# Optimization experiments

Hardware: AMD Instinct MI355X
Metric: run time of the kernel (lower is better)

The kernel has to match this reference:

```python
import jax, jax.numpy as jnp
import numpy as np
import math

HEAD_SIZE = 128
N_EMBED = 2048
B, T = 4, 4096
TOP_K_RATIO = 0.1


def setup_inputs() -> dict:
    key = jax.random.key(0)
    k1, k2, k3, k4 = jax.random.split(key, 4)
    index = jax.random.normal(k1, (B, T, N_EMBED), dtype=jnp.float32)
    s = 1.0 / math.sqrt(N_EMBED)
    Wq = jax.random.normal(k2, (N_EMBED, HEAD_SIZE), dtype=jnp.float32) * s
    Wk = jax.random.normal(k3, (N_EMBED, HEAD_SIZE), dtype=jnp.float32) * s
    Wv = jax.random.normal(k4, (N_EMBED, HEAD_SIZE), dtype=jnp.float32) * s
    return {"index": index, "Wq": Wq, "Wk": Wk, "Wv": Wv}


def reference(index, Wq, Wk, Wv):
    # memory = index (self-attention case)
    Bv, Tv, _ = index.shape
    top_k = int(TOP_K_RATIO * Tv)  # 409

    q = index @ Wq  # [B, T, D]
    k = index @ Wk
    v = index @ Wv

    q_norms = jnp.linalg.norm(q, axis=-1)  # [B, T]
    _, top_idx = jax.lax.top_k(q_norms, top_k)  # [B, K]

    idx = top_idx[..., None]  # [B, K, 1]
    q_topk = jnp.take_along_axis(q, idx, axis=1)  # [B, K, D]
    k_topk = jnp.take_along_axis(k, idx, axis=1)
    v_topk = jnp.take_along_axis(v, idx, axis=1)

    w = jnp.einsum('bid,bjd->bij', q_topk, k_topk) / math.sqrt(HEAD_SIZE)
    # eval mode: no causal mask (only applied in training), dropout = identity
    w = jax.nn.softmax(w, axis=-1)  # stable softmax (internal max subtraction)
    out_topk = w @ v_topk  # [B, K, D]

    batch_idx = jnp.arange(Bv)[:, None]  # [B, 1]
    output = jnp.zeros((Bv, Tv, HEAD_SIZE), dtype=out_topk.dtype)
    output = output.at[batch_idx, top_idx].add(out_topk)  # scatter_add (indices unique)
    return output
```

## Files before the change

### kernel.cpp

```cpp
#include <hip/hip_runtime.h>
#include <hip/hip_bf16.h>

#define NB 4
#define NT 4096
#define NC 2048
#define ND 128
#define NK 409
#define KPAD 416
#define NM (NB * NK)

typedef __attribute__((ext_vector_type(8))) short short8;
typedef __attribute__((ext_vector_type(4))) float f32x4;

union S8U { short8 v; ushort u[8]; };

__device__ __forceinline__ void split2(float x, ushort& h, ushort& l) {
    union { float f; unsigned u; } a; a.f = x;
    unsigned r = a.u + 0x7FFFu + ((a.u >> 16) & 1u);
    h = (ushort)(r >> 16);
    union { unsigned u; float f; } hb; hb.u = ((unsigned)h) << 16;
    float res = x - hb.f;
    union { float f; unsigned u; } b; b.f = res;
    unsigned r2 = b.u + 0x7FFFu + ((b.u >> 16) & 1u);
    l = (ushort)(r2 >> 16);
}

__device__ __forceinline__ uint4 pack8(const ushort* s) {
    uint4 v;
    v.x = (unsigned)s[0] | ((unsigned)s[1] << 16);
    v.y = (unsigned)s[2] | ((unsigned)s[3] << 16);
    v.z = (unsigned)s[4] | ((unsigned)s[5] << 16);
    v.w = (unsigned)s[6] | ((unsigned)s[7] << 16);
    return v;
}

__device__ __forceinline__ int slotOf(int n, int lq) {
    return n * 4 + ((lq + (n >> 1)) & 3);
}

__global__ __launch_bounds__(256) void bconv_tiles(
    const float* __restrict__ W, ushort* __restrict__ Bt)
{
    const int kt = blockIdx.x;
    const int t = threadIdx.x;
    const int n = t & 127;
    const int lq0 = (t >> 7) * 2;
    #pragma unroll
    for (int e = 0; e < 2; ++e) {
        int lq = lq0 + e;
        ushort h[8], l[8];
        #pragma unroll
        for (int j = 0; j < 8; ++j) {
            float x = W[(size_t)(kt * 32 + lq * 8 + j) * ND + n];
            split2(x, h[j], l[j]);
        }
        int slot = slotOf(n, lq);
        *(uint4*)&Bt[((size_t)(kt * 2 + 0) * 512 + slot) * 8] = pack8(h);
        *(uint4*)&Bt[((size_t)(kt * 2 + 1) * 512 + slot) * 8] = pack8(l);
    }
}

#define QSTEP(BHC, BLC, BHN, BLN, KT)                                         \
    {                                                                         \
        short8 ah, al;                                                        \
        {                                                                     \
            S8U H, L;                                                         \
            float xs[8] = {fa0.x, fa0.y, fa0.z, fa0.w,                        \
                           fa1.x, fa1.y, fa1.z, fa1.w};                       \
            _Pragma("unroll")                                                 \
            for (int j = 0; j < 8; ++j) split2(xs[j], H.u[j], L.u[j]);        \
            ah = H.v; al = L.v;                                               \
        }                                                                     \
        const int ktn = ((KT) + 1 < KITER) ? (KT) + 1 : (KT);                 \
        const ushort* gbn = Bt + (size_t)(kt0 + ktn) * 8192;                  \
        _Pragma("unroll")                                                     \
        for (int ni = 0; ni < 8; ++ni) {                                      \
            BHN[ni] = *(const short8*)(gbn + boff[ni]);                       \
            BLN[ni] = *(const short8*)(gbn + 4096 + boff[ni]);                \
        }                                                                     \
        fa0 = *(const float4*)(arow + ktn * 32);                              \
        fa1 = *(const float4*)(arow + ktn * 32 + 4);                          \
        _Pragma("unroll")                                                     \
        for (int ni = 0; ni < 8; ++ni) {                                      \
            acc[ni] = __builtin_amdgcn_mfma_f32_16x16x32_bf16(ah, BHC[ni], acc[ni], 0, 0, 0); \
            acc[ni] = __builtin_amdgcn_mfma_f32_16x16x32_bf16(ah, BLC[ni], acc[ni], 0, 0, 0); \
            acc[ni] = __builtin_amdgcn_mfma_f32_16x16x32_bf16(al, BHC[ni], acc[ni], 0, 0, 0); \
        }                                                                     \
    }

#define QSPLIT 2
__global__ __launch_bounds__(512, 4) void qgemm_v7(
    const float* __restrict__ A, const ushort* __restrict__ Bt,
    float* __restrict__ q1, float* __restrict__ q2)
{
    __shared__ __align__(16) float RED[4][64][32];

    const int tid = threadIdx.x;
    const int w = tid >> 6, lane = tid & 63;
    const int rg = w & 3, kh = w >> 2;
    const int lrow = lane & 15, lq = lane >> 4;
    const int m0 = blockIdx.x * 64;
    const int KITER = 16;
    const int kt0 = (blockIdx.y * 2 + kh) * 16;
    const int kb = blockIdx.y * 1024 + kh * 512;

    const float* arow = A + (size_t)(m0 + rg * 16 + lrow) * NC + kb + lq * 8;

    int boff[8];
    #pragma unroll
    for (int ni = 0; ni < 8; ++ni)
        boff[ni] = slotOf(ni * 16 + lrow, lq) * 8;

    f32x4 acc[8];
    #pragma unroll
    for (int i = 0; i < 8; ++i) acc[i] = (f32x4){0.f, 0.f, 0.f, 0.f};

    short8 bhA[8], blA[8], bhB[8], blB[8];
    {
        const ushort* gb = Bt + (size_t)kt0 * 8192;
        #pragma unroll
        for (int ni = 0; ni < 8; ++ni) {
            bhA[ni] = *(const short8*)(gb + boff[ni]);
            blA[ni] = *(const short8*)(gb + 4096 + boff[ni]);
        }
    }
    float4 fa0 = *(const float4*)(arow + 0);
    float4 fa1 = *(const float4*)(arow + 4);

    for (int kt = 0; kt < KITER; kt += 2) {
        QSTEP(bhA, blA, bhB, blB, kt);
        QSTEP(bhB, blB, bhA, blA, kt + 1);
    }

    if (kh == 1) {
        #pragma unroll
        for (int c = 0; c < 8; ++c) {
            int ch = (c + lane) & 7;
            *(f32x4*)&RED[rg][lane][ch * 4] = acc[ch];
        }
    }
    __syncthreads();
    if (kh == 0) {
        #pragma unroll
        for (int c = 0; c < 8; ++c) {
            int ch = (c + lane) & 7;
            f32x4 o = *(const f32x4*)&RED[rg][lane][ch * 4];
            acc[ch][0] += o[0]; acc[ch][1] += o[1];
            acc[ch][2] += o[2]; acc[ch][3] += o[3];
        }
        float* __restrict__ qd = blockIdx.y ? q2 : q1;
        #pragma unroll
        for (int ni = 0; ni < 8; ++ni) {
            const int col = ni * 16 + lrow;
            #pragma unroll
            for (int r = 0; r < 4; ++r) {
                const int grow = m0 + rg * 16 + lq * 4 + r;
                qd[(size_t)grow * ND + col] = acc[ni][r];
            }
        }
    }
}

#define KVSPLIT 8
__global__ __launch_bounds__(256) void kvgemm_v5(
    const float* __restrict__ X, const ushort* __restrict__ Bkt,
    const ushort* __restrict__ Bvt, const int* __restrict__ topi,
    float* __restrict__ ktop, float* __restrict__ vtop)
{
    const int tid = threadIdx.x;
    const int w = tid >> 6, lane = tid & 63;
    const int lrow = lane & 15, lq = lane >> 4;
    const int m0 = blockIdx.x * 64;
    const int KITER = (NC / KVSPLIT) / 32;
    const int kt0 = blockIdx.y * KITER;
    const int kb = blockIdx.y * (NC / KVSPLIT);
    const ushort* __restrict__ Bt = blockIdx.z ? Bvt : Bkt;

    const int gi = m0 + w * 16 + lrow;
    const int giC = gi < NM ? gi : NM - 1;
    const int b = giC / NK, ii = giC % NK;
    const int src = topi[b * KPAD + ii];
    const float* arow = X + ((size_t)b * NT + src) * NC + kb + lq * 8;

    int boff[8];
    #pragma unroll
    for (int ni = 0; ni < 8; ++ni)
        boff[ni] = slotOf(ni * 16 + lrow, lq) * 8;

    f32x4 acc[8];
    #pragma unroll
    for (int i = 0; i < 8; ++i) acc[i] = (f32x4){0.f, 0.f, 0.f, 0.f};

    short8 bhA[8], blA[8], bhB[8], blB[8];
    {
        const ushort* gb = Bt + (size_t)kt0 * 8192;
        #pragma unroll
        for (int ni = 0; ni < 8; ++ni) {
            bhA[ni] = *(const short8*)(gb + boff[ni]);
            blA[ni] = *(const short8*)(gb + 4096 + boff[ni]);
        }
    }
    float4 fa0 = *(const float4*)(arow + 0);
    float4 fa1 = *(const float4*)(arow + 4);

    for (int kt = 0; kt < KITER; kt += 2) {
        QSTEP(bhA, blA, bhB, blB, kt);
        QSTEP(bhB, blB, bhA, blA, kt + 1);
    }

    float* __restrict__ dst = blockIdx.z ? vtop : ktop;
    #pragma unroll
    for (int ni = 0; ni < 8; ++ni) {
        const int col = ni * 16 + lrow;
        #pragma unroll
        for (int r = 0; r < 4; ++r) {
            const int grow = m0 + w * 16 + lq * 4 + r;
            if (grow < NM)
                atomicAdd(&dst[(size_t)grow * ND + col], acc[ni][r]);
        }
    }
}

__global__ __launch_bounds__(256) void qnorm_kernel(
    float* __restrict__ q1, const float* __restrict__ q2, float* __restrict__ qn)
{
    const int wv = (blockIdx.x * 256 + threadIdx.x) >> 6;
    const int lane = threadIdx.x & 63;
    float* r1 = q1 + (size_t)wv * ND;
    const float* r2 = q2 + (size_t)wv * ND;
    float a = r1[lane] + r2[lane];
    float b = r1[lane + 64] + r2[lane + 64];
    r1[lane] = a;
    r1[lane + 64] = b;
    float s = a * a + b * b;
    #pragma unroll
    for (int off = 32; off > 0; off >>= 1) s += __shfl_xor(s, off);
    if (lane == 0) qn[wv] = sqrtf(s);
}

__global__ __launch_bounds__(256) void topk_kernel(
    const float* __restrict__ qn, int* __restrict__ topi, int* __restrict__ cnt)
{
    __shared__ int rs[4][64];
    const int b = blockIdx.y;
    const int is = threadIdx.x & 63;
    const int i = blockIdx.x * 64 + is;
    const int chunk = threadIdx.x >> 6;
    const float vi = qn[(size_t)b * NT + i];
    const float4* qv = (const float4*)(qn + (size_t)b * NT + chunk * 1024);
    int rank = 0;
    #pragma unroll 4
    for (int j4 = 0; j4 < 256; ++j4) {
        float4 v = qv[j4];
        int j = chunk * 1024 + j4 * 4;
        rank += (v.x > vi || (v.x == vi && (j + 0) < i)) ? 1 : 0;
        rank += (v.y > vi || (v.y == vi && (j + 1) < i)) ? 1 : 0;
        rank += (v.z > vi || (v.z == vi && (j + 2) < i)) ? 1 : 0;
        rank += (v.w > vi || (v.w == vi && (j + 3) < i)) ? 1 : 0;
    }
    rs[chunk][is] = rank;
    __syncthreads();
    if (threadIdx.x < 64) {
        int rk = rs[0][threadIdx.x] + rs[1][threadIdx.x] + rs[2][threadIdx.x] + rs[3][threadIdx.x];
        if (rk < NK) {
            int p = atomicAdd(&cnt[b], 1);
            topi[b * KPAD + p] = blockIdx.x * 64 + threadIdx.x;
        }
    }
}

__global__ __launch_bounds__(256) void attn_kernel(
    const float* __restrict__ q, const float* __restrict__ ktop,
    const float* __restrict__ vtop, const int* __restrict__ topi,
    float* __restrict__ out)
{
    __shared__ float qs[ND];
    __shared__ float ss[KPAD];
    __shared__ float red[256];
    __shared__ float pv[2][ND];
    const int bi = blockIdx.x;
    const int b = bi / NK, i = bi % NK;
    const int t = threadIdx.x;
    const int row = topi[b * KPAD + i];
    if (t < ND) qs[t] = q[((size_t)b * NT + row) * ND + t];
    __syncthreads();

    const float scale = 0.08838834764831844f;
    float mymax = -1e30f;
    #pragma unroll
    for (int rep = 0; rep < 2; ++rep) {
        int j = t + rep * 256;
        if (j < NK) {
            const float4* kr = (const float4*)(ktop + ((size_t)b * NK + j) * ND);
            const float4* q4 = (const float4*)qs;
            float s = 0.f;
            #pragma unroll
            for (int dd = 0; dd < 32; ++dd) {
                float4 a = q4[dd], kv = kr[dd];
                s += a.x * kv.x + a.y * kv.y + a.z * kv.z + a.w * kv.w;
            }
            s *= scale;
            ss[j] = s;
            mymax = fmaxf(mymax, s);
        }
    }
    red[t] = mymax;
    __syncthreads();
    for (int off = 128; off > 0; off >>= 1) {
        if (t < off) red[t] = fmaxf(red[t], red[t + off]);
        __syncthreads();
    }
    const float mx = red[0];
    __syncthreads();

    float mysum = 0.f;
    #pragma unroll
    for (int rep = 0; rep < 2; ++rep) {
        int j = t + rep * 256;
        if (j < NK) {
            float p = __expf(ss[j] - mx);
            ss[j] = p;
            mysum += p;
        }
    }
    red[t] = mysum;
    __syncthreads();
    for (int off = 128; off > 0; off >>= 1) {
        if (t < off) red[t] += red[t + off];
        __syncthreads();
    }
    const float inv = 1.f / red[0];

    const int col = t & (ND - 1), half = t >> 7;
    float o = 0.f;
    #pragma unroll 4
    for (int j = half; j < NK; j += 2)
        o = fmaf(ss[j], vtop[((size_t)b * NK + j) * ND + col], o);
    pv[half][col] = o;
    __syncthreads();
    if (t < ND)
        out[((size_t)b * NT + row) * ND + t] = (pv[0][t] + pv[1][t]) * inv;
}

extern "C" void kernel_launch(void* const* d_in, const int* in_sizes, int n_in,
                              void* d_out, int out_size, void* d_ws, size_t ws_size,
                              hipStream_t stream)
{
    const float* index = (const float*)d_in[0];
    const float* Wq = (const float*)d_in[1];
    const float* Wk = (const float*)d_in[2];
    const float* Wv = (const float*)d_in[3];
    float* out = (float*)d_out;

    char* ws = (char*)d_ws;
    float*  q1   = (float*)(ws);
    float*  qn   = (float*)(ws + 8388608);
    int*    topi = (int*)  (ws + 8454144);
    int*    cnt  = (int*)  (ws + 8462336);
    ushort* Bqt  = (ushort*)(ws + 8462592);
    float*  ktop = (float*)(ws + 8462592);
    float*  vtop = (float*)(ws + 9300224);

    float*  q2  = (float*)d_out;
    ushort* Bkt = (ushort*)d_out;
    ushort* Bvt = (ushort*)((char*)d_out + 1048576);

    hipMemsetAsync(cnt, 0, NB * sizeof(int), stream);

    bconv_tiles<<<dim3(64), dim3(256), 0, stream>>>(Wq, Bqt);
    qgemm_v7<<<dim3(NB * NT / 64, QSPLIT), dim3(512), 0, stream>>>(index, Bqt, q1, q2);
    qnorm_kernel<<<dim3(NB * NT / 4), dim3(256), 0, stream>>>(q1, q2, qn);
    topk_kernel<<<dim3(NT / 64, NB), dim3(256), 0, stream>>>(qn, topi, cnt);
    bconv_tiles<<<dim3(64), dim3(256), 0, stream>>>(Wk, Bkt);
    bconv_tiles<<<dim3(64), dim3(256), 0, stream>>>(Wv, Bvt);
    hipMemsetAsync(ktop, 0, 2 * 837632, stream);
    kvgemm_v5<<<dim3((NM + 63) / 64, KVSPLIT, 2), dim3(256), 0, stream>>>(
        index, Bkt, Bvt, topi, ktop, vtop);
    hipMemsetAsync(d_out, 0, (size_t)out_size * sizeof(float), stream);
    attn_kernel<<<dim3(NM), dim3(256), 0, stream>>>(q1, ktop, vtop, topi, out);
}
```

Baseline: 396.1 us.

## Split GEMM tiles across N halves instead of K halves, dropping LDS reduction

The Q and KV GEMM kernels now assign waves to 32-row by 64-column tiles, splitting the N dimension across waves instead of splitting K within a block. This removes the shared-memory reduction and __syncthreads in the Q GEMM, and halves the per-wave B register footprint. The cost is that each A row fragment (fp32 loaded from global and split into bf16 hi/lo) is now loaded and converted twice, once per N-half wave. Block count doubles with smaller blocks.

```diff
diff --git a/kernel.cpp b/kernel.cpp
--- a/kernel.cpp
+++ b/kernel.cpp
@@ -74,14 +74,14 @@
         const int ktn = ((KT) + 1 < KITER) ? (KT) + 1 : (KT);                 \
         const ushort* gbn = Bt + (size_t)(kt0 + ktn) * 8192;                  \
         _Pragma("unroll")                                                     \
-        for (int ni = 0; ni < 8; ++ni) {                                      \
+        for (int ni = 0; ni < 4; ++ni) {                                      \
             BHN[ni] = *(const short8*)(gbn + boff[ni]);                       \
             BLN[ni] = *(const short8*)(gbn + 4096 + boff[ni]);                \
         }                                                                     \
         fa0 = *(const float4*)(arow + ktn * 32);                              \
         fa1 = *(const float4*)(arow + ktn * 32 + 4);                          \
         _Pragma("unroll")                                                     \
-        for (int ni = 0; ni < 8; ++ni) {                                      \
+        for (int ni = 0; ni < 4; ++ni) {                                      \
             acc[ni] = __builtin_amdgcn_mfma_f32_16x16x32_bf16(ah, BHC[ni], acc[ni], 0, 0, 0); \
             acc[ni] = __builtin_amdgcn_mfma_f32_16x16x32_bf16(ah, BLC[ni], acc[ni], 0, 0, 0); \
             acc[ni] = __builtin_amdgcn_mfma_f32_16x16x32_bf16(al, BHC[ni], acc[ni], 0, 0, 0); \
@@ -89,37 +89,35 @@
     }
 
 #define QSPLIT 2
-__global__ __launch_bounds__(512, 4) void qgemm_v7(
+__global__ __launch_bounds__(256) void qgemm_v9(
     const float* __restrict__ A, const ushort* __restrict__ Bt,
     float* __restrict__ q1, float* __restrict__ q2)
 {
-    __shared__ __align__(16) float RED[4][64][32];
-
     const int tid = threadIdx.x;
     const int w = tid >> 6, lane = tid & 63;
-    const int rg = w & 3, kh = w >> 2;
+    const int rg = w & 1, nh = w >> 1;
     const int lrow = lane & 15, lq = lane >> 4;
-    const int m0 = blockIdx.x * 64;
-    const int KITER = 16;
-    const int kt0 = (blockIdx.y * 2 + kh) * 16;
-    const int kb = blockIdx.y * 1024 + kh * 512;
+    const int m0 = blockIdx.x * 32;
+    const int KITER = (NC / QSPLIT) / 32;
+    const int kt0 = blockIdx.y * KITER;
+    const int kb = blockIdx.y * (NC / QSPLIT);
 
     const float* arow = A + (size_t)(m0 + rg * 16 + lrow) * NC + kb + lq * 8;
 
-    int boff[8];
-    #pragma unroll
-    for (int ni = 0; ni < 8; ++ni)
-        boff[ni] = slotOf(ni * 16 + lrow, lq) * 8;
-
-    f32x4 acc[8];
-    #pragma unroll
-    for (int i = 0; i < 8; ++i) acc[i] = (f32x4){0.f, 0.f, 0.f, 0.f};
-
-    short8 bhA[8], blA[8], bhB[8], blB[8];
+    int boff[4];
+    #pragma unroll
+    for (int ni = 0; ni < 4; ++ni)
+        boff[ni] = slotOf(nh * 64 + ni * 16 + lrow, lq) * 8;
+
+    f32x4 acc[4];
+    #pragma unroll
+    for (int i = 0; i < 4; ++i) acc[i] = (f32x4){0.f, 0.f, 0.f, 0.f};
+
+    short8 bhA[4], blA[4], bhB[4], blB[4];
     {
         const ushort* gb = Bt + (size_t)kt0 * 8192;
         #pragma unroll
-        for (int ni = 0; ni < 8; ++ni) {
+        for (int ni = 0; ni < 4; ++ni) {
             bhA[ni] = *(const short8*)(gb + boff[ni]);
             blA[ni] = *(const short8*)(gb + 4096 + boff[ni]);
         }
@@ -132,70 +130,54 @@
         QSTEP(bhB, blB, bhA, blA, kt + 1);
     }
 
-    if (kh == 1) {
-        #pragma unroll
-        for (int c = 0; c < 8; ++c) {
-            int ch = (c + lane) & 7;
-            *(f32x4*)&RED[rg][lane][ch * 4] = acc[ch];
-        }
-    }
-    __syncthreads();
-    if (kh == 0) {
-        #pragma unroll
-        for (int c = 0; c < 8; ++c) {
-            int ch = (c + lane) & 7;
-            f32x4 o = *(const f32x4*)&RED[rg][lane][ch * 4];
-            acc[ch][0] += o[0]; acc[ch][1] += o[1];
-            acc[ch][2] += o[2]; acc[ch][3] += o[3];
-        }
-        float* __restrict__ qd = blockIdx.y ? q2 : q1;
-        #pragma unroll
-        for (int ni = 0; ni < 8; ++ni) {
-            const int col = ni * 16 + lrow;
-            #pragma unroll
-            for (int r = 0; r < 4; ++r) {
-                const int grow = m0 + rg * 16 + lq * 4 + r;
-                qd[(size_t)grow * ND + col] = acc[ni][r];
-            }
+    float* __restrict__ qd = blockIdx.y ? q2 : q1;
+    #pragma unroll
+    for (int ni = 0; ni < 4; ++ni) {
+        const int col = nh * 64 + ni * 16 + lrow;
+        #pragma unroll
+        for (int r = 0; r < 4; ++r) {
+            const int grow = m0 + rg * 16 + lq * 4 + r;
+            qd[(size_t)grow * ND + col] = acc[ni][r];
         }
     }
 }
 
 #define KVSPLIT 8
-__global__ __launch_bounds__(256) void kvgemm_v5(
+__global__ __launch_bounds__(256) void kvgemm_v9(
     const float* __restrict__ X, const ushort* __restrict__ Bkt,
     const ushort* __restrict__ Bvt, const int* __restrict__ topi,
     float* __restrict__ ktop, float* __restrict__ vtop)
 {
     const int tid = threadIdx.x;
     const int w = tid >> 6, lane = tid & 63;
+    const int rg = w & 1, nh = w >> 1;
     const int lrow = lane & 15, lq = lane >> 4;
-    const int m0 = blockIdx.x * 64;
+    const int m0 = blockIdx.x * 32;
     const int KITER = (NC / KVSPLIT) / 32;
     const int kt0 = blockIdx.y * KITER;
     const int kb = blockIdx.y * (NC / KVSPLIT);
     const ushort* __restrict__ Bt = blockIdx.z ? Bvt : Bkt;
 
-    const int gi = m0 + w * 16 + lrow;
+    const int gi = m0 + rg * 16 + lrow;
     const int giC = gi < NM ? gi : NM - 1;
     const int b = giC / NK, ii = giC % NK;
     const int src = topi[b * KPAD + ii];
     const float* arow = X + ((size_t)b * NT + src) * NC + kb + lq * 8;
 
-    int boff[8];
-    #pragma unroll
-    for (int ni = 0; ni < 8; ++ni)
-        boff[ni] = slotOf(ni * 16 + lrow, lq) * 8;
-
-    f32x4 acc[8];
-    #pragma unroll
-    for (int i = 0; i < 8; ++i) acc[i] = (f32x4){0.f, 0.f, 0.f, 0.f};
-
-    short8 bhA[8], blA[8], bhB[8], blB[8];
+    int boff[4];
+    #pragma unroll
+    for (int ni = 0; ni < 4; ++ni)
+        boff[ni] = slotOf(nh * 64 + ni * 16 + lrow, lq) * 8;
+
+    f32x4 acc[4];
+    #pragma unroll
+    for (int i = 0; i < 4; ++i) acc[i] = (f32x4){0.f, 0.f, 0.f, 0.f};
+
+    short8 bhA[4], blA[4], bhB[4], blB[4];
     {
         const ushort* gb = Bt + (size_t)kt0 * 8192;
         #pragma unroll
-        for (int ni = 0; ni < 8; ++ni) {
+        for (int ni = 0; ni < 4; ++ni) {
             bhA[ni] = *(const short8*)(gb + boff[ni]);
             blA[ni] = *(const short8*)(gb + 4096 + boff[ni]);
         }
@@ -210,11 +192,11 @@
 
     float* __restrict__ dst = blockIdx.z ? vtop : ktop;
     #pragma unroll
-    for (int ni = 0; ni < 8; ++ni) {
-        const int col = ni * 16 + lrow;
+    for (int ni = 0; ni < 4; ++ni) {
+        const int col = nh * 64 + ni * 16 + lrow;
         #pragma unroll
         for (int r = 0; r < 4; ++r) {
-            const int grow = m0 + w * 16 + lq * 4 + r;
+            const int grow = m0 + rg * 16 + lq * 4 + r;
             if (grow < NM)
                 atomicAdd(&dst[(size_t)grow * ND + col], acc[ni][r]);
         }
@@ -368,13 +350,13 @@
     hipMemsetAsync(cnt, 0, NB * sizeof(int), stream);
 
     bconv_tiles<<<dim3(64), dim3(256), 0, stream>>>(Wq, Bqt);
-    qgemm_v7<<<dim3(NB * NT / 64, QSPLIT), dim3(512), 0, stream>>>(index, Bqt, q1, q2);
+    qgemm_v9<<<dim3(NB * NT / 32, QSPLIT), dim3(256), 0, stream>>>(index, Bqt, q1, q2);
     qnorm_kernel<<<dim3(NB * NT / 4), dim3(256), 0, stream>>>(q1, q2, qn);
     topk_kernel<<<dim3(NT / 64, NB), dim3(256), 0, stream>>>(qn, topi, cnt);
     bconv_tiles<<<dim3(64), dim3(256), 0, stream>>>(Wk, Bkt);
     bconv_tiles<<<dim3(64), dim3(256), 0, stream>>>(Wv, Bvt);
     hipMemsetAsync(ktop, 0, 2 * 837632, stream);
-    kvgemm_v5<<<dim3((NM + 63) / 64, KVSPLIT, 2), dim3(256), 0, stream>>>(
+    kvgemm_v9<<<dim3((NM + 31) / 32, KVSPLIT, 2), dim3(256), 0, stream>>>(
         index, Bkt, Bvt, topi, ktop, vtop);
     hipMemsetAsync(d_out, 0, (size_t)out_size * sizeof(float), stream);
     attn_kernel<<<dim3(NM), dim3(256), 0, stream>>>(q1, ktop, vtop, topi, out);
```

Measured after the change: 389.5 us. Within noise of the previous version (-1.7%).

## Drop intra-block K-split in Q GEMM and issue A loads before B loads

Applied to the files above, without the earlier changes.

The Q projection kernel moves from 512-thread blocks, where two wave groups split the K range and reduce through shared memory, to 256-thread blocks in which each wave runs the full 1024-wide K half on its own. This removes the LDS reduction and the __syncthreads, at the cost of a longer serial K loop per wave with the same grid size. The shared pipelining macro also now issues the fp32 A-row prefetch ahead of the B-tile loads, so the activation stream, which is the longer-latency load, starts earlier. This applies to both the Q and K/V GEMMs.

```diff
diff --git a/kernel.cpp b/kernel.cpp
--- a/kernel.cpp
+++ b/kernel.cpp
@@ -72,14 +72,14 @@
             ah = H.v; al = L.v;                                               \
         }                                                                     \
         const int ktn = ((KT) + 1 < KITER) ? (KT) + 1 : (KT);                 \
+        fa0 = *(const float4*)(arow + ktn * 32);        \
+        fa1 = *(const float4*)(arow + ktn * 32 + 4);                          \
         const ushort* gbn = Bt + (size_t)(kt0 + ktn) * 8192;                  \
         _Pragma("unroll")                                                     \
         for (int ni = 0; ni < 8; ++ni) {                                      \
             BHN[ni] = *(const short8*)(gbn + boff[ni]);                       \
             BLN[ni] = *(const short8*)(gbn + 4096 + boff[ni]);                \
         }                                                                     \
-        fa0 = *(const float4*)(arow + ktn * 32);                              \
-        fa1 = *(const float4*)(arow + ktn * 32 + 4);                          \
         _Pragma("unroll")                                                     \
         for (int ni = 0; ni < 8; ++ni) {                                      \
             acc[ni] = __builtin_amdgcn_mfma_f32_16x16x32_bf16(ah, BHC[ni], acc[ni], 0, 0, 0); \
@@ -89,22 +89,19 @@
     }
 
 #define QSPLIT 2
-__global__ __launch_bounds__(512, 4) void qgemm_v7(
+__global__ __launch_bounds__(256) void qgemm_v11(
     const float* __restrict__ A, const ushort* __restrict__ Bt,
     float* __restrict__ q1, float* __restrict__ q2)
 {
-    __shared__ __align__(16) float RED[4][64][32];
-
     const int tid = threadIdx.x;
     const int w = tid >> 6, lane = tid & 63;
-    const int rg = w & 3, kh = w >> 2;
     const int lrow = lane & 15, lq = lane >> 4;
     const int m0 = blockIdx.x * 64;
-    const int KITER = 16;
-    const int kt0 = (blockIdx.y * 2 + kh) * 16;
-    const int kb = blockIdx.y * 1024 + kh * 512;
-
-    const float* arow = A + (size_t)(m0 + rg * 16 + lrow) * NC + kb + lq * 8;
+    const int KITER = (NC / QSPLIT) / 32;
+    const int kt0 = blockIdx.y * KITER;
+    const int kb = blockIdx.y * (NC / QSPLIT);
+
+    const float* arow = A + (size_t)(m0 + w * 16 + lrow) * NC + kb + lq * 8;
 
     int boff[8];
     #pragma unroll
@@ -115,6 +112,8 @@
     #pragma unroll
     for (int i = 0; i < 8; ++i) acc[i] = (f32x4){0.f, 0.f, 0.f, 0.f};
 
+    float4 fa0 = *(const float4*)(arow + 0);
+    float4 fa1 = *(const float4*)(arow + 4);
     short8 bhA[8], blA[8], bhB[8], blB[8];
     {
         const ushort* gb = Bt + (size_t)kt0 * 8192;
@@ -124,45 +123,26 @@
             blA[ni] = *(const short8*)(gb + 4096 + boff[ni]);
         }
     }
-    float4 fa0 = *(const float4*)(arow + 0);
-    float4 fa1 = *(const float4*)(arow + 4);
 
     for (int kt = 0; kt < KITER; kt += 2) {
         QSTEP(bhA, blA, bhB, blB, kt);
         QSTEP(bhB, blB, bhA, blA, kt + 1);
     }
 
-    if (kh == 1) {
-        #pragma unroll
-        for (int c = 0; c < 8; ++c) {
-            int ch = (c + lane) & 7;
-            *(f32x4*)&RED[rg][lane][ch * 4] = acc[ch];
-        }
-    }
-    __syncthreads();
-    if (kh == 0) {
-        #pragma unroll
-        for (int c = 0; c < 8; ++c) {
-            int ch = (c + lane) & 7;
-            f32x4 o = *(const f32x4*)&RED[rg][lane][ch * 4];
-            acc[ch][0] += o[0]; acc[ch][1] += o[1];
-            acc[ch][2] += o[2]; acc[ch][3] += o[3];
-        }
-        float* __restrict__ qd = blockIdx.y ? q2 : q1;
-        #pragma unroll
-        for (int ni = 0; ni < 8; ++ni) {
-            const int col = ni * 16 + lrow;
-            #pragma unroll
-            for (int r = 0; r < 4; ++r) {
-                const int grow = m0 + rg * 16 + lq * 4 + r;
-                qd[(size_t)grow * ND + col] = acc[ni][r];
-            }
+    float* __restrict__ qd = blockIdx.y ? q2 : q1;
+    #pragma unroll
+    for (int ni = 0; ni < 8; ++ni) {
+        const int col = ni * 16 + lrow;
+        #pragma unroll
+        for (int r = 0; r < 4; ++r) {
+            const int grow = m0 + w * 16 + lq * 4 + r;
+            qd[(size_t)grow * ND + col] = acc[ni][r];
         }
     }
 }
 
 #define KVSPLIT 8
-__global__ __launch_bounds__(256) void kvgemm_v5(
+__global__ __launch_bounds__(256) void kvgemm_v11(
     const float* __restrict__ X, const ushort* __restrict__ Bkt,
     const ushort* __restrict__ Bvt, const int* __restrict__ topi,
     float* __restrict__ ktop, float* __restrict__ vtop)
@@ -191,6 +171,8 @@
     #pragma unroll
     for (int i = 0; i < 8; ++i) acc[i] = (f32x4){0.f, 0.f, 0.f, 0.f};
 
+    float4 fa0 = *(const float4*)(arow + 0);
+    float4 fa1 = *(const float4*)(arow + 4);
     short8 bhA[8], blA[8], bhB[8], blB[8];
     {
         const ushort* gb = Bt + (size_t)kt0 * 8192;
@@ -200,8 +182,6 @@
             blA[ni] = *(const short8*)(gb + 4096 + boff[ni]);
         }
     }
-    float4 fa0 = *(const float4*)(arow + 0);
-    float4 fa1 = *(const float4*)(arow + 4);
 
     for (int kt = 0; kt < KITER; kt += 2) {
         QSTEP(bhA, blA, bhB, blB, kt);
@@ -368,13 +348,13 @@
     hipMemsetAsync(cnt, 0, NB * sizeof(int), stream);
 
     bconv_tiles<<<dim3(64), dim3(256), 0, stream>>>(Wq, Bqt);
-    qgemm_v7<<<dim3(NB * NT / 64, QSPLIT), dim3(512), 0, stream>>>(index, Bqt, q1, q2);
+    qgemm_v11<<<dim3(NB * NT / 64, QSPLIT), dim3(256), 0, stream>>>(index, Bqt, q1, q2);
     qnorm_kernel<<<dim3(NB * NT / 4), dim3(256), 0, stream>>>(q1, q2, qn);
     topk_kernel<<<dim3(NT / 64, NB), dim3(256), 0, stream>>>(qn, topi, cnt);
     bconv_tiles<<<dim3(64), dim3(256), 0, stream>>>(Wk, Bkt);
     bconv_tiles<<<dim3(64), dim3(256), 0, stream>>>(Wv, Bvt);
     hipMemsetAsync(ktop, 0, 2 * 837632, stream);
-    kvgemm_v5<<<dim3((NM + 63) / 64, KVSPLIT, 2), dim3(256), 0, stream>>>(
+    kvgemm_v11<<<dim3((NM + 63) / 64, KVSPLIT, 2), dim3(256), 0, stream>>>(
         index, Bkt, Bvt, topi, ktop, vtop);
     hipMemsetAsync(d_out, 0, (size_t)out_size * sizeof(float), stream);
     attn_kernel<<<dim3(NM), dim3(256), 0, stream>>>(q1, ktop, vtop, topi, out);
```

New measurement: 369.7 us. -6.7%, faster.

## Swap split-K strategies between Q and KV GEMMs and fuse K/V weight conversion

Applied to the files above, without the earlier changes.

The Q projection GEMM drops its in-block two-wave-group K split and LDS reduction and runs as a plain 256-thread kernel that splits K across two grid slices. The gathered K/V GEMM moves the opposite way: a 512-thread block splits K internally and reduces through LDS, and the grid split drops from 8 to 4, which halves the number of global atomicAdds. The two K and V weight-conversion launches are merged into one 2D launch. The A-row loads are also issued before the B-tile loads inside the pipeline step.

```diff
diff --git a/kernel.cpp b/kernel.cpp
--- a/kernel.cpp
+++ b/kernel.cpp
@@ -38,11 +38,9 @@
     return n * 4 + ((lq + (n >> 1)) & 3);
 }
 
-__global__ __launch_bounds__(256) void bconv_tiles(
-    const float* __restrict__ W, ushort* __restrict__ Bt)
-{
-    const int kt = blockIdx.x;
-    const int t = threadIdx.x;
+__device__ __forceinline__ void bconv_body(
+    const float* __restrict__ W, ushort* __restrict__ Bt, int kt, int t)
+{
     const int n = t & 127;
     const int lq0 = (t >> 7) * 2;
     #pragma unroll
@@ -58,6 +56,21 @@
         *(uint4*)&Bt[((size_t)(kt * 2 + 0) * 512 + slot) * 8] = pack8(h);
         *(uint4*)&Bt[((size_t)(kt * 2 + 1) * 512 + slot) * 8] = pack8(l);
     }
+}
+
+__global__ __launch_bounds__(256) void bconv_tiles(
+    const float* __restrict__ W, ushort* __restrict__ Bt)
+{
+    bconv_body(W, Bt, blockIdx.x, threadIdx.x);
+}
+
+__global__ __launch_bounds__(256) void bconv2_tiles(
+    const float* __restrict__ Wk, const float* __restrict__ Wv,
+    ushort* __restrict__ Bkt, ushort* __restrict__ Bvt)
+{
+    const float* W = blockIdx.y ? Wv : Wk;
+    ushort* Bt = blockIdx.y ? Bvt : Bkt;
+    bconv_body(W, Bt, blockIdx.x, threadIdx.x);
 }
 
 #define QSTEP(BHC, BLC, BHN, BLN, KT)                                         \
@@ -72,14 +85,14 @@
             ah = H.v; al = L.v;                                               \
         }                                                                     \
         const int ktn = ((KT) + 1 < KITER) ? (KT) + 1 : (KT);                 \
+        fa0 = *(const float4*)(arow + ktn * 32);                              \
+        fa1 = *(const float4*)(arow + ktn * 32 + 4);                          \
         const ushort* gbn = Bt + (size_t)(kt0 + ktn) * 8192;                  \
         _Pragma("unroll")                                                     \
         for (int ni = 0; ni < 8; ++ni) {                                      \
             BHN[ni] = *(const short8*)(gbn + boff[ni]);                       \
             BLN[ni] = *(const short8*)(gbn + 4096 + boff[ni]);                \
         }                                                                     \
-        fa0 = *(const float4*)(arow + ktn * 32);                              \
-        fa1 = *(const float4*)(arow + ktn * 32 + 4);                          \
         _Pragma("unroll")                                                     \
         for (int ni = 0; ni < 8; ++ni) {                                      \
             acc[ni] = __builtin_amdgcn_mfma_f32_16x16x32_bf16(ah, BHC[ni], acc[ni], 0, 0, 0); \
@@ -89,9 +102,63 @@
     }
 
 #define QSPLIT 2
-__global__ __launch_bounds__(512, 4) void qgemm_v7(
+__global__ __launch_bounds__(256) void qgemm_v11(
     const float* __restrict__ A, const ushort* __restrict__ Bt,
     float* __restrict__ q1, float* __restrict__ q2)
+{
+    const int tid = threadIdx.x;
+    const int w = tid >> 6, lane = tid & 63;
+    const int lrow = lane & 15, lq = lane >> 4;
+    const int m0 = blockIdx.x * 64;
+    const int KITER = (NC / QSPLIT) / 32;
+    const int kt0 = blockIdx.y * KITER;
+    const int kb = blockIdx.y * (NC / QSPLIT);
+
+    const float* arow = A + (size_t)(m0 + w * 16 + lrow) * NC + kb + lq * 8;
+
+    int boff[8];
+    #pragma unroll
+    for (int ni = 0; ni < 8; ++ni)
+        boff[ni] = slotOf(ni * 16 + lrow, lq) * 8;
+
+    f32x4 acc[8];
+    #pragma unroll
+    for (int i = 0; i < 8; ++i) acc[i] = (f32x4){0.f, 0.f, 0.f, 0.f};
+
+    float4 fa0 = *(const float4*)(arow + 0);
+    float4 fa1 = *(const float4*)(arow + 4);
+    short8 bhA[8], blA[8], bhB[8], blB[8];
+    {
+        const ushort* gb = Bt + (size_t)kt0 * 8192;
+        #pragma unroll
+        for (int ni = 0; ni < 8; ++ni) {
+            bhA[ni] = *(const short8*)(gb + boff[ni]);
+            blA[ni] = *(const short8*)(gb + 4096 + boff[ni]);
+        }
+    }
+
+    for (int kt = 0; kt < KITER; kt += 2) {
+        QSTEP(bhA, blA, bhB, blB, kt);
+        QSTEP(bhB, blB, bhA, blA, kt + 1);
+    }
+
+    float* __restrict__ qd = blockIdx.y ? q2 : q1;
+    #pragma unroll
+    for (int ni = 0; ni < 8; ++ni) {
+        const int col = ni * 16 + lrow;
+        #pragma unroll
+        for (int r = 0; r < 4; ++r) {
+            const int grow = m0 + w * 16 + lq * 4 + r;
+            qd[(size_t)grow * ND + col] = acc[ni][r];
+        }
+    }
+}
+
+#define KVSPLIT 4
+__global__ __launch_bounds__(512, 2) void kvgemm_v12(
+    const float* __restrict__ X, const ushort* __restrict__ Bkt,
+    const ushort* __restrict__ Bvt, const int* __restrict__ topi,
+    float* __restrict__ ktop, float* __restrict__ vtop)
 {
     __shared__ __align__(16) float RED[4][64][32];
 
@@ -100,11 +167,16 @@
     const int rg = w & 3, kh = w >> 2;
     const int lrow = lane & 15, lq = lane >> 4;
     const int m0 = blockIdx.x * 64;
-    const int KITER = 16;
-    const int kt0 = (blockIdx.y * 2 + kh) * 16;
-    const int kb = blockIdx.y * 1024 + kh * 512;
-
-    const float* arow = A + (size_t)(m0 + rg * 16 + lrow) * NC + kb + lq * 8;
+    const int KITER = 8;
+    const int kt0 = blockIdx.y * 16 + kh * 8;
+    const int kb = blockIdx.y * 512 + kh * 256;
+    const ushort* __restrict__ Bt = blockIdx.z ? Bvt : Bkt;
+
+    const int gi = m0 + rg * 16 + lrow;
+    const int giC = gi < NM ? gi : NM - 1;
+    const int b = giC / NK, ii = giC % NK;
+    const int src = topi[b * KPAD + ii];
+    const float* arow = X + ((size_t)b * NT + src) * NC + kb + lq * 8;
 
     int boff[8];
     #pragma unroll
@@ -115,6 +187,8 @@
     #pragma unroll
     for (int i = 0; i < 8; ++i) acc[i] = (f32x4){0.f, 0.f, 0.f, 0.f};
 
+    float4 fa0 = *(const float4*)(arow + 0);
+    float4 fa1 = *(const float4*)(arow + 4);
     short8 bhA[8], blA[8], bhB[8], blB[8];
     {
         const ushort* gb = Bt + (size_t)kt0 * 8192;
@@ -124,8 +198,6 @@
             blA[ni] = *(const short8*)(gb + 4096 + boff[ni]);
         }
     }
-    float4 fa0 = *(const float4*)(arow + 0);
-    float4 fa1 = *(const float4*)(arow + 4);
 
     for (int kt = 0; kt < KITER; kt += 2) {
         QSTEP(bhA, blA, bhB, blB, kt);
@@ -148,75 +220,16 @@
             acc[ch][0] += o[0]; acc[ch][1] += o[1];
             acc[ch][2] += o[2]; acc[ch][3] += o[3];
         }
-        float* __restrict__ qd = blockIdx.y ? q2 : q1;
+        float* __restrict__ dst = blockIdx.z ? vtop : ktop;
         #pragma unroll
         for (int ni = 0; ni < 8; ++ni) {
             const int col = ni * 16 + lrow;
             #pragma unroll
             for (int r = 0; r < 4; ++r) {
                 const int grow = m0 + rg * 16 + lq * 4 + r;
-                qd[(size_t)grow * ND + col] = acc[ni][r];
+                if (grow < NM)
+                    atomicAdd(&dst[(size_t)grow * ND + col], acc[ni][r]);
             }
-        }
-    }
-}
-
-#define KVSPLIT 8
-__global__ __launch_bounds__(256) void kvgemm_v5(
-    const float* __restrict__ X, const ushort* __restrict__ Bkt,
-    const ushort* __restrict__ Bvt, const int* __restrict__ topi,
-    float* __restrict__ ktop, float* __restrict__ vtop)
-{
-    const int tid = threadIdx.x;
-    const int w = tid >> 6, lane = tid & 63;
-    const int lrow = lane & 15, lq = lane >> 4;
-    const int m0 = blockIdx.x * 64;
-    const int KITER = (NC / KVSPLIT) / 32;
-    const int kt0 = blockIdx.y * KITER;
-    const int kb = blockIdx.y * (NC / KVSPLIT);
-    const ushort* __restrict__ Bt = blockIdx.z ? Bvt : Bkt;
-
-    const int gi = m0 + w * 16 + lrow;
-    const int giC = gi < NM ? gi : NM - 1;
-    const int b = giC / NK, ii = giC % NK;
-    const int src = topi[b * KPAD + ii];
-    const float* arow = X + ((size_t)b * NT + src) * NC + kb + lq * 8;
-
-    int boff[8];
-    #pragma unroll
-    for (int ni = 0; ni < 8; ++ni)
-        boff[ni] = slotOf(ni * 16 + lrow, lq) * 8;
-
-    f32x4 acc[8];
-    #pragma unroll
-    for (int i = 0; i < 8; ++i) acc[i] = (f32x4){0.f, 0.f, 0.f, 0.f};
-
-    short8 bhA[8], blA[8], bhB[8], blB[8];
-    {
-        const ushort* gb = Bt + (size_t)kt0 * 8192;
-        #pragma unroll
-        for (int ni = 0; ni < 8; ++ni) {
-            bhA[ni] = *(const short8*)(gb + boff[ni]);
-            blA[ni] = *(const short8*)(gb + 4096 + boff[ni]);
-        }
-    }
-    float4 fa0 = *(const float4*)(arow + 0);
-    float4 fa1 = *(const float4*)(arow + 4);
-
-    for (int kt = 0; kt < KITER; kt += 2) {
-        QSTEP(bhA, blA, bhB, blB, kt);
-        QSTEP(bhB, blB, bhA, blA, kt + 1);
-    }
-
-    float* __restrict__ dst = blockIdx.z ? vtop : ktop;
-    #pragma unroll
-    for (int ni = 0; ni < 8; ++ni) {
-        const int col = ni * 16 + lrow;
-        #pragma unroll
-        for (int r = 0; r < 4; ++r) {
-            const int grow = m0 + w * 16 + lq * 4 + r;
-            if (grow < NM)
-                atomicAdd(&dst[(size_t)grow * ND + col], acc[ni][r]);
         }
     }
 }
@@ -368,13 +381,12 @@
     hipMemsetAsync(cnt, 0, NB * sizeof(int), stream);
 
     bconv_tiles<<<dim3(64), dim3(256), 0, stream>>>(Wq, Bqt);
-    qgemm_v7<<<dim3(NB * NT / 64, QSPLIT), dim3(512), 0, stream>>>(index, Bqt, q1, q2);
+    qgemm_v11<<<dim3(NB * NT / 64, QSPLIT), dim3(256), 0, stream>>>(index, Bqt, q1, q2);
     qnorm_kernel<<<dim3(NB * NT / 4), dim3(256), 0, stream>>>(q1, q2, qn);
     topk_kernel<<<dim3(NT / 64, NB), dim3(256), 0, stream>>>(qn, topi, cnt);
-    bconv_tiles<<<dim3(64), dim3(256), 0, stream>>>(Wk, Bkt);
-    bconv_tiles<<<dim3(64), dim3(256), 0, stream>>>(Wv, Bvt);
+    bconv2_tiles<<<dim3(64, 2), dim3(256), 0, stream>>>(Wk, Wv, Bkt, Bvt);
     hipMemsetAsync(ktop, 0, 2 * 837632, stream);
-    kvgemm_v5<<<dim3((NM + 63) / 64, KVSPLIT, 2), dim3(256), 0, stream>>>(
+    kvgemm_v12<<<dim3((NM + 63) / 64, KVSPLIT, 2), dim3(512), 0, stream>>>(
         index, Bkt, Bvt, topi, ktop, vtop);
     hipMemsetAsync(d_out, 0, (size_t)out_size * sizeof(float), stream);
     attn_kernel<<<dim3(NM), dim3(256), 0, stream>>>(q1, ktop, vtop, topi, out);
```

New measurement: 390.9 us. No clear change (-1.3%).
